# Optimization experiments

Measured on AMD Instinct MI355X. Metric: run time of the kernel, lower is better.

The kernel has to match this reference:

```python
import jax, jax.numpy as jnp
import numpy as np

B, T, C = 8, 2048, 1024


def setup_inputs() -> dict:
    key = jax.random.key(0)
    ks = jax.random.split(key, 7)
    s = 0.02  # typical init scale for weights
    return {
        "x": jax.random.normal(ks[0], (B, T, C), jnp.float32),
        "wq": jax.random.normal(ks[1], (C, C), jnp.float32) * s,
        "bq": jax.random.normal(ks[2], (C,), jnp.float32) * s,
        "wk": jax.random.normal(ks[3], (C, C), jnp.float32) * s,
        "bk": jax.random.normal(ks[4], (C,), jnp.float32) * s,
        "wv": jax.random.normal(ks[5], (C, C), jnp.float32) * s,
        "bv": jax.random.normal(ks[6], (C,), jnp.float32) * s,
    }


def reference(x, wq, bq, wk, bk, wv, bv):
    # x: [B, T, C]; torch Linear stores weight as [out, in] -> x @ W.T + b
    Bx, Tx, Cx = x.shape
    Q = x @ wq.T + bq  # [B, T, C]
    K = x @ wk.T + bk
    V = x @ wv.T + bv
    # NOTE: source computes K @ Q^T (keys index rows, queries index columns)
    scores = jnp.einsum("btc,bsc->bts", K, Q) / jnp.sqrt(jnp.float32(Cx))  # [B, T, T]
    causal = jnp.tril(jnp.ones((Tx, Tx), dtype=bool))  # mask==0 above diagonal
    scores = jnp.where(causal, scores, -jnp.inf)
    # torch masked_fill with a (1,1,T,T) mask broadcasts scores to (1,B,T,T)
    scores = scores[None]  # [1, B, T, T]
    w = jax.nn.softmax(scores, axis=-1)
    out = jnp.einsum("abts,bsc->abtc", w, V)  # [1, B, T, C]
    return out
```

## Files before the change

kernel.cpp:

```cpp
#include <hip/hip_runtime.h>
#include <stdint.h>

typedef unsigned short u16;
typedef __attribute__((ext_vector_type(8))) __bf16 bf16x8;
typedef __attribute__((ext_vector_type(4))) float f32x4;

#define DEVI __device__ __forceinline__

DEVI u16 f32_to_bf16(float f) {
  uint32_t u = __builtin_bit_cast(uint32_t, f);
  u += 0x7FFFu + ((u >> 16) & 1u);
  return (u16)(u >> 16);
}

DEVI void gl2lds16(const void* g, void* l) {
  __builtin_amdgcn_global_load_lds(
      (const __attribute__((address_space(1))) void*)g,
      (__attribute__((address_space(3))) void*)l, 16, 0, 0);
}

#define S_BATCH 2228224

__global__ void cast_f32_to_bf16_kernel(const float* __restrict__ src,
                                        u16* __restrict__ dst, int n4) {
  int i = blockIdx.x * blockDim.x + threadIdx.x;
  const int stride = gridDim.x * blockDim.x;
  for (; i < n4; i += stride) {
    const float4 v = ((const float4*)src)[i];
    ushort4 o;
    o.x = f32_to_bf16(v.x);
    o.y = f32_to_bf16(v.y);
    o.z = f32_to_bf16(v.z);
    o.w = f32_to_bf16(v.w);
    ((ushort4*)dst)[i] = o;
  }
}

__global__ void cast_w_kernel(const float* __restrict__ wq,
                              const float* __restrict__ wk,
                              const float* __restrict__ wv,
                              u16* __restrict__ wb, float* __restrict__ sums) {
  const int z = blockIdx.y;
  if (z == 3) {
    int i = blockIdx.x * blockDim.x + threadIdx.x;
    if (i < 4096) ((float4*)sums)[i] = (float4){0.f, 0.f, 0.f, 0.f};
    return;
  }
  const float* src = (z == 0) ? wq : (z == 1) ? wk : wv;
  u16* dst = wb + (size_t)z * 1048576;
  int i = blockIdx.x * blockDim.x + threadIdx.x;
  const int stride = gridDim.x * blockDim.x;
  for (; i < 262144; i += stride) {
    const float4 v = ((const float4*)src)[i];
    ushort4 o;
    o.x = f32_to_bf16(v.x);
    o.y = f32_to_bf16(v.y);
    o.z = f32_to_bf16(v.z);
    o.w = f32_to_bf16(v.w);
    ((ushort4*)dst)[i] = o;
  }
}

__global__ __launch_bounds__(512, 2) void qkv_kernel(
    const u16* __restrict__ xb, const u16* __restrict__ wb,
    const float* __restrict__ bq, const float* __restrict__ bk,
    const float* __restrict__ bv, u16* __restrict__ Qb, u16* __restrict__ Kb,
    u16* __restrict__ Vt) {
  __shared__ __align__(16) u16 lds[65536];

  const int id = blockIdx.x;
  const int wg = (id & 7) * 96 + (id >> 3);
  const int g = wg >> 3, u = wg & 7;
  const int z = g >> 5;
  const int tp = g & 31;
  const int tmt = tp * 2 + (u >> 2);
  const int tct = u & 3;

  int m0, n0;
  const u16* Aptr;
  const u16* Bptr;
  if (z < 2) {
    m0 = tct * 256;
    n0 = tmt * 256;
    Aptr = wb + (size_t)z * 1048576 + (size_t)m0 * 1024;
    Bptr = xb + (size_t)n0 * 1024;
  } else {
    m0 = tmt * 256;
    n0 = tct * 256;
    Aptr = xb + (size_t)m0 * 1024;
    Bptr = wb + (size_t)2 * 1048576 + (size_t)n0 * 1024;
  }

  const int tid = threadIdx.x;
  const int srow = tid >> 3;
  const int sgrp = ((tid & 7) - srow) & 7;
  const u16* Ag = Aptr + (size_t)srow * 1024 + sgrp * 8;
  const u16* Bg = Bptr + (size_t)srow * 1024 + sgrp * 8;
  char* ldsDst = (char*)lds + tid * 16;

#define ST_A0(kt) do { const u16* s_ = Ag + (kt) * 64;           char* d_ = ldsDst + (((kt) & 1) * 65536);         gl2lds16(s_, d_); gl2lds16(s_ + 65536, d_ + 8192); } while (0)
#define ST_A1(kt) do { const u16* s_ = Ag + 131072 + (kt) * 64;  char* d_ = ldsDst + (((kt) & 1) * 65536) + 16384; gl2lds16(s_, d_); gl2lds16(s_ + 65536, d_ + 8192); } while (0)
#define ST_B0(kt) do { const u16* s_ = Bg + (kt) * 64;           char* d_ = ldsDst + (((kt) & 1) * 65536) + 32768; gl2lds16(s_, d_); gl2lds16(s_ + 65536, d_ + 8192); } while (0)
#define ST_B1(kt) do { const u16* s_ = Bg + 131072 + (kt) * 64;  char* d_ = ldsDst + (((kt) & 1) * 65536) + 49152; gl2lds16(s_, d_); gl2lds16(s_ + 65536, d_ + 8192); } while (0)

  ST_A0(0); ST_B0(0); ST_B1(0); ST_A1(0);
  ST_A0(1); ST_B0(1); ST_B1(1);

  const int lane = tid & 63, wid = tid >> 6;
  const int wr = wid >> 2, wc = wid & 3;
  const int l15 = lane & 15, quad = lane >> 4;

  int aoff[4][2], boff[2][2];
#pragma unroll
  for (int i_ = 0; i_ < 4; ++i_) {
    const int arow = wr * 64 + i_ * 16 + l15;
#pragma unroll
    for (int k_ = 0; k_ < 2; ++k_)
      aoff[i_][k_] = arow * 64 + ((k_ * 4 + quad + arow) & 7) * 8;
  }
#pragma unroll
  for (int j_ = 0; j_ < 2; ++j_) {
    const int brow = wc * 32 + j_ * 16 + l15;
#pragma unroll
    for (int k_ = 0; k_ < 2; ++k_)
      boff[j_][k_] = brow * 64 + ((k_ * 4 + quad + brow) & 7) * 8;
  }

  f32x4 acc[2][2][4][2];
#pragma unroll
  for (int a_ = 0; a_ < 2; ++a_)
#pragma unroll
    for (int b_ = 0; b_ < 2; ++b_)
#pragma unroll
      for (int i_ = 0; i_ < 4; ++i_)
#pragma unroll
        for (int j_ = 0; j_ < 2; ++j_)
          acc[a_][b_][i_][j_] = (f32x4){0.f, 0.f, 0.f, 0.f};

  bf16x8 af[4][2], bfr[2][2][2];

#define LOADA(qm, buf) do { const u16* p_ = lds + (buf) * 32768 + (qm) * 8192; \
  _Pragma("unroll") for (int i_ = 0; i_ < 4; ++i_) \
  _Pragma("unroll") for (int k_ = 0; k_ < 2; ++k_) \
    af[i_][k_] = *(const bf16x8*)(p_ + aoff[i_][k_]); } while (0)
#define LOADB(qn, buf) do { const u16* p_ = lds + (buf) * 32768 + 16384 + (qn) * 8192; \
  _Pragma("unroll") for (int j_ = 0; j_ < 2; ++j_) \
  _Pragma("unroll") for (int k_ = 0; k_ < 2; ++k_) \
    bfr[qn][j_][k_] = *(const bf16x8*)(p_ + boff[j_][k_]); } while (0)
#define MMA(qm, qn) do { \
  _Pragma("unroll") for (int i_ = 0; i_ < 4; ++i_) \
  _Pragma("unroll") for (int j_ = 0; j_ < 2; ++j_) \
  _Pragma("unroll") for (int k_ = 0; k_ < 2; ++k_) \
    acc[qm][qn][i_][j_] = __builtin_amdgcn_mfma_f32_16x16x32_bf16( \
        af[i_][k_], bfr[qn][j_][k_], acc[qm][qn][i_][j_], 0, 0, 0); } while (0)

#define BAR __builtin_amdgcn_s_barrier()
#define WLG0 asm volatile("s_waitcnt lgkmcnt(0)")
#define WLG8 asm volatile("s_waitcnt lgkmcnt(8)")
#define PRIO1 __builtin_amdgcn_s_setprio(1)
#define PRIO0 __builtin_amdgcn_s_setprio(0)
#define WVM6 asm volatile("s_waitcnt vmcnt(6)" ::: "memory")
#define WVM0 asm volatile("s_waitcnt vmcnt(0)" ::: "memory")

  WVM6;
  BAR;

#pragma unroll 1
  for (int it = 0; it < 7; ++it) {
    const int j0 = 2 * it;
    LOADA(0, 0); LOADB(0, 0); ST_A1(j0 + 1); WLG8;
    BAR; WLG0; PRIO1; MMA(0, 0); PRIO0; BAR;
    LOADB(1, 0); ST_A0(j0 + 2);
    BAR; WLG0; PRIO1; MMA(0, 1); PRIO0; BAR;
    LOADA(1, 0); ST_B0(j0 + 2);
    BAR; WLG0; PRIO1; MMA(1, 1); PRIO0; BAR;
    ST_B1(j0 + 2);
    BAR; PRIO1; MMA(1, 0); PRIO0;
    WVM6;
    BAR;
    LOADA(0, 1); LOADB(0, 1); ST_A1(j0 + 2); WLG8;
    BAR; WLG0; PRIO1; MMA(0, 0); PRIO0; BAR;
    LOADB(1, 1); ST_A0(j0 + 3);
    BAR; WLG0; PRIO1; MMA(0, 1); PRIO0; BAR;
    LOADA(1, 1); ST_B0(j0 + 3);
    BAR; WLG0; PRIO1; MMA(1, 1); PRIO0; BAR;
    ST_B1(j0 + 3);
    BAR; PRIO1; MMA(1, 0); PRIO0;
    WVM6;
    BAR;
  }
  {
    LOADA(0, 0); LOADB(0, 0); ST_A1(15); WLG8;
    BAR; WLG0; PRIO1; MMA(0, 0); PRIO0; BAR;
    LOADB(1, 0);
    BAR; WLG0; PRIO1; MMA(0, 1); PRIO0; BAR;
    LOADA(1, 0);
    BAR; WLG0; PRIO1; MMA(1, 1); PRIO0; BAR;
    BAR; PRIO1; MMA(1, 0); PRIO0;
    WVM0;
    BAR;
    LOADA(0, 1); LOADB(0, 1); WLG8;
    BAR; WLG0; PRIO1; MMA(0, 0); PRIO0; BAR;
    LOADB(1, 1);
    BAR; WLG0; PRIO1; MMA(0, 1); PRIO0; BAR;
    LOADA(1, 1);
    BAR; WLG0; PRIO1; MMA(1, 1); PRIO0; BAR;
    PRIO1; MMA(1, 0); PRIO0;
    BAR;
  }

  if (z < 2) {
    const float* bias = (z == 0) ? bq : bk;
    u16* Out = (z == 0) ? Qb : Kb;
#pragma unroll
    for (int th = 0; th < 2; ++th) {
      if (th) __syncthreads();
#pragma unroll
      for (int qm = 0; qm < 2; ++qm)
#pragma unroll
        for (int i_ = 0; i_ < 4; ++i_) {
          const int c = qm * 128 + wr * 64 + i_ * 16 + quad * 4;
          const float4 b4 = *(const float4*)(bias + m0 + c);
#pragma unroll
          for (int j_ = 0; j_ < 2; ++j_) {
            const int row = wc * 32 + j_ * 16 + l15;
            ushort4 o;
            o.x = f32_to_bf16(acc[qm][th][i_][j_][0] + b4.x);
            o.y = f32_to_bf16(acc[qm][th][i_][j_][1] + b4.y);
            o.z = f32_to_bf16(acc[qm][th][i_][j_][2] + b4.z);
            o.w = f32_to_bf16(acc[qm][th][i_][j_][3] + b4.w);
            *(ushort4*)(lds + row * 264 + c) = o;
          }
        }
      __syncthreads();
#pragma unroll
      for (int p = 0; p < 8; ++p) {
        const int row = p * 16 + (tid >> 5);
        const int c0 = (tid & 31) * 8;
        const uint4 v = *(const uint4*)(lds + row * 264 + c0);
        *(uint4*)(Out + (size_t)(n0 + th * 128 + row) * 1024 + m0 + c0) = v;
      }
    }
  } else {
    const int b = m0 >> 11;
    const int t0b = m0 & 2047;
    u16* Out = Vt + (size_t)b * 2097152;
#pragma unroll
    for (int th = 0; th < 2; ++th) {
      if (th) __syncthreads();
#pragma unroll
      for (int j_ = 0; j_ < 2; ++j_) {
        const int row = wc * 32 + j_ * 16 + l15;
        const float bb = bv[n0 + th * 128 + row];
#pragma unroll
        for (int qm = 0; qm < 2; ++qm)
#pragma unroll
          for (int i_ = 0; i_ < 4; ++i_) {
            const int c = qm * 128 + wr * 64 + i_ * 16 + quad * 4;
            ushort4 o;
            o.x = f32_to_bf16(acc[qm][th][i_][j_][0] + bb);
            o.y = f32_to_bf16(acc[qm][th][i_][j_][1] + bb);
            o.z = f32_to_bf16(acc[qm][th][i_][j_][2] + bb);
            o.w = f32_to_bf16(acc[qm][th][i_][j_][3] + bb);
            *(ushort4*)(lds + row * 264 + c) = o;
          }
      }
      __syncthreads();
#pragma unroll
      for (int p = 0; p < 8; ++p) {
        const int row = p * 16 + (tid >> 5);
        const int c0 = (tid & 31) * 8;
        const uint4 v = *(const uint4*)(lds + row * 264 + c0);
        *(uint4*)(Out + (size_t)(n0 + th * 128 + row) * 2048 + t0b + c0) = v;
      }
    }
  }
#undef ST_A0
#undef ST_A1
#undef ST_B0
#undef ST_B1
#undef LOADA
#undef LOADB
#undef MMA
#undef BAR
#undef WLG0
#undef WLG8
#undef PRIO1
#undef PRIO0
#undef WVM6
#undef WVM0
}

__global__ __launch_bounds__(512, 2) void score_kernel(const u16* __restrict__ Kb,
                                                       const u16* __restrict__ Qb,
                                                       u16* __restrict__ Spk,
                                                       float* __restrict__ sums) {
  __shared__ __align__(16) u16 lds[49152];

  const int id = blockIdx.x;
  const int b = id & 7;
  const int l = id >> 3;
  int k = (int)((sqrtf(4.f * l + 1.f) - 1.f) * 0.5f);
  if (k * (k + 1) > l) --k;
  if ((k + 1) * (k + 2) <= l) ++k;
  const int off = l - k * (k + 1);
  const int hi = (off >= (k + 1));
  const int rt = 2 * k + hi;
  const int ct = off - (hi ? (k + 1) : 0);
  const bool maskT = (ct == k);

  const int tid = threadIdx.x;
  const int srow = tid >> 3;
  const int sgrp = ((tid & 7) - srow) & 7;
  const u16* A = Qb + ((size_t)b * 2048 + ct * 256) * 1024;
  const u16* B = Kb + ((size_t)b * 2048 + rt * 128) * 1024;
  const u16* Ag = A + (size_t)srow * 1024 + sgrp * 8;
  const u16* Bg = B + (size_t)srow * 1024 + sgrp * 8;
  char* ldsDst = (char*)lds + tid * 16;

#define ST_A0(kt) do { const u16* s_ = Ag + (kt) * 64;           char* d_ = ldsDst + (((kt) & 1) * 49152);         gl2lds16(s_, d_); gl2lds16(s_ + 65536, d_ + 8192); } while (0)
#define ST_A1(kt) do { const u16* s_ = Ag + 131072 + (kt) * 64;  char* d_ = ldsDst + (((kt) & 1) * 49152) + 16384; gl2lds16(s_, d_); gl2lds16(s_ + 65536, d_ + 8192); } while (0)
#define ST_B(kt)  do { const u16* s_ = Bg + (kt) * 64;           char* d_ = ldsDst + (((kt) & 1) * 49152) + 32768; gl2lds16(s_, d_); gl2lds16(s_ + 65536, d_ + 8192); } while (0)

  ST_A0(0); ST_B(0); ST_A1(0);
  ST_A0(1); ST_B(1);

  const int lane = tid & 63, wid = tid >> 6;
  const int wr = wid >> 2, wc = wid & 3;
  const int l15 = lane & 15, quad = lane >> 4;

  int aoff[4][2], boff[2][2];
#pragma unroll
  for (int i_ = 0; i_ < 4; ++i_) {
    const int arow = wr * 64 + i_ * 16 + l15;
#pragma unroll
    for (int k_ = 0; k_ < 2; ++k_)
      aoff[i_][k_] = arow * 64 + ((k_ * 4 + quad + arow) & 7) * 8;
  }
#pragma unroll
  for (int j_ = 0; j_ < 2; ++j_) {
    const int brow = wc * 32 + j_ * 16 + l15;
#pragma unroll
    for (int k_ = 0; k_ < 2; ++k_)
      boff[j_][k_] = brow * 64 + ((k_ * 4 + quad + brow) & 7) * 8;
  }

  f32x4 acc[2][4][2];
#pragma unroll
  for (int q_ = 0; q_ < 2; ++q_)
#pragma unroll
    for (int i_ = 0; i_ < 4; ++i_)
#pragma unroll
      for (int j_ = 0; j_ < 2; ++j_)
        acc[q_][i_][j_] = (f32x4){0.f, 0.f, 0.f, 0.f};

  bf16x8 af[4][2], bfr[2][2];

#define SLOADA(qm, buf) do { const u16* p_ = lds + (buf) * 24576 + (qm) * 8192; \
  _Pragma("unroll") for (int i_ = 0; i_ < 4; ++i_) \
  _Pragma("unroll") for (int k_ = 0; k_ < 2; ++k_) \
    af[i_][k_] = *(const bf16x8*)(p_ + aoff[i_][k_]); } while (0)
#define SLOADB(buf) do { const u16* p_ = lds + (buf) * 24576 + 16384; \
  _Pragma("unroll") for (int j_ = 0; j_ < 2; ++j_) \
  _Pragma("unroll") for (int k_ = 0; k_ < 2; ++k_) \
    bfr[j_][k_] = *(const bf16x8*)(p_ + boff[j_][k_]); } while (0)
#define SMMA(qm) do { \
  _Pragma("unroll") for (int i_ = 0; i_ < 4; ++i_) \
  _Pragma("unroll") for (int j_ = 0; j_ < 2; ++j_) \
  _Pragma("unroll") for (int k_ = 0; k_ < 2; ++k_) \
    acc[qm][i_][j_] = __builtin_amdgcn_mfma_f32_16x16x32_bf16( \
        af[i_][k_], bfr[j_][k_], acc[qm][i_][j_], 0, 0, 0); } while (0)

#define BAR __builtin_amdgcn_s_barrier()
#define WLG0 asm volatile("s_waitcnt lgkmcnt(0)")
#define PRIO1 __builtin_amdgcn_s_setprio(1)
#define PRIO0 __builtin_amdgcn_s_setprio(0)
#define WVM4 asm volatile("s_waitcnt vmcnt(4)" ::: "memory")
#define WVM0 asm volatile("s_waitcnt vmcnt(0)" ::: "memory")

  WVM4;
  BAR;

#pragma unroll 1
  for (int it = 0; it < 7; ++it) {
    const int j0 = 2 * it;
    SLOADA(0, 0); SLOADB(0); ST_A1(j0 + 1);
    BAR; WLG0; PRIO1; SMMA(0); PRIO0; BAR;
    SLOADA(1, 0); ST_A0(j0 + 2); ST_B(j0 + 2);
    BAR; WLG0; PRIO1; SMMA(1); PRIO0;
    WVM4;
    BAR;
    SLOADA(0, 1); SLOADB(1); ST_A1(j0 + 2);
    BAR; WLG0; PRIO1; SMMA(0); PRIO0; BAR;
    SLOADA(1, 1); ST_A0(j0 + 3); ST_B(j0 + 3);
    BAR; WLG0; PRIO1; SMMA(1); PRIO0;
    WVM4;
    BAR;
  }
  {
    SLOADA(0, 0); SLOADB(0); ST_A1(15);
    BAR; WLG0; PRIO1; SMMA(0); PRIO0; BAR;
    SLOADA(1, 0);
    BAR; WLG0; PRIO1; SMMA(1); PRIO0;
    WVM0;
    BAR;
    SLOADA(0, 1); SLOADB(1);
    BAR; WLG0; PRIO1; SMMA(0); PRIO0; BAR;
    SLOADA(1, 1);
    BAR; WLG0; PRIO1; SMMA(1); PRIO0; BAR;
  }

  const int moff = (rt & 1) * 128;
  float sj[2] = {0.f, 0.f};
#pragma unroll
  for (int qm = 0; qm < 2; ++qm)
#pragma unroll
    for (int i_ = 0; i_ < 4; ++i_) {
      const int s0 = qm * 128 + wr * 64 + i_ * 16 + quad * 4;
#pragma unroll
      for (int j_ = 0; j_ < 2; ++j_) {
        const int t = wc * 32 + j_ * 16 + l15;
        ushort4 o;
        float e[4];
#pragma unroll
        for (int r = 0; r < 4; ++r) {
          float v = __expf(acc[qm][i_][j_][r] * 0.03125f);
          if (maskT && (s0 + r) > (t + moff)) v = 0.f;
          e[r] = v;
          sj[j_] += v;
        }
        o.x = f32_to_bf16(e[0]);
        o.y = f32_to_bf16(e[1]);
        o.z = f32_to_bf16(e[2]);
        o.w = f32_to_bf16(e[3]);
        *(ushort4*)(lds + t * 264 + s0) = o;
      }
    }
#pragma unroll
  for (int j_ = 0; j_ < 2; ++j_) {
    float v = sj[j_];
    v += __shfl_xor(v, 16);
    v += __shfl_xor(v, 32);
    if (quad == 0)
      atomicAdd(&sums[(size_t)b * 2048 + rt * 128 + wc * 32 + j_ * 16 + l15], v);
  }
  __syncthreads();
  const int ld = (rt + 1) * 128;
  const int nc = ld - ct * 256;
  u16* Out = Spk + (size_t)b * S_BATCH + (size_t)(rt * (rt + 1) / 2) * 16384 +
             ct * 256;
  if (nc >= 256) {
#pragma unroll
    for (int p = 0; p < 8; ++p) {
      const int row = p * 16 + (tid >> 5);
      const int c0 = (tid & 31) * 8;
      const uint4 v = *(const uint4*)(lds + row * 264 + c0);
      *(uint4*)(Out + (size_t)row * ld + c0) = v;
    }
  } else {
#pragma unroll
    for (int p = 0; p < 4; ++p) {
      const int row = p * 32 + (tid >> 4);
      const int c0 = (tid & 15) * 8;
      const uint4 v = *(const uint4*)(lds + row * 264 + c0);
      *(uint4*)(Out + (size_t)row * ld + c0) = v;
    }
  }
#undef ST_A0
#undef ST_A1
#undef ST_B
#undef SLOADA
#undef SLOADB
#undef SMMA
#undef BAR
#undef WLG0
#undef PRIO1
#undef PRIO0
#undef WVM4
#undef WVM0
}

__global__ __launch_bounds__(512, 2) void pv_kernel(const u16* __restrict__ Spk,
                                                    const u16* __restrict__ Vt,
                                                    const float* __restrict__ sums,
                                                    float* __restrict__ Out) {
  __shared__ __align__(16) u16 lds[49152];

  const int id = blockIdx.x;
  const int hf = id >> 8;
  const int rr_ = id & 255;
  const int rt = hf ? (rr_ >> 5) : 15 - (rr_ >> 5);
  const int ct = (rr_ >> 3) & 3;
  const int b = rr_ & 7;

  const int ldb = (rt + 1) * 128;
  const int nk2 = rt + 1;

  const int tid = threadIdx.x;
  const int srow = tid >> 3;
  const int sgrp = ((tid & 7) - srow) & 7;
  const u16* A = Vt + ((size_t)b * 1024 + ct * 256) * 2048;
  const u16* B = Spk + (size_t)b * S_BATCH +
                 (size_t)(rt * (rt + 1) / 2) * 16384;
  const u16* Ag = A + (size_t)srow * 2048 + sgrp * 8;
  const u16* Bg = B + (size_t)srow * ldb + sgrp * 8;
  char* ldsDst = (char*)lds + tid * 16;

#define ST_A0(kt) do { const u16* s_ = Ag + (kt) * 64;            char* d_ = ldsDst + (((kt) & 1) * 49152);         gl2lds16(s_, d_); gl2lds16(s_ + 131072, d_ + 8192); } while (0)
#define ST_A1(kt) do { const u16* s_ = Ag + 262144 + (kt) * 64;   char* d_ = ldsDst + (((kt) & 1) * 49152) + 16384; gl2lds16(s_, d_); gl2lds16(s_ + 131072, d_ + 8192); } while (0)
#define ST_B(kt)  do { const u16* s_ = Bg + (kt) * 64;            char* d_ = ldsDst + (((kt) & 1) * 49152) + 32768; gl2lds16(s_, d_); gl2lds16(s_ + (size_t)64 * ldb, d_ + 8192); } while (0)

  ST_A0(0); ST_B(0); ST_A1(0);
  ST_A0(1); ST_B(1);

  const int lane = tid & 63, wid = tid >> 6;
  const int wr = wid >> 2, wc = wid & 3;
  const int l15 = lane & 15, quad = lane >> 4;

  int aoff[4][2], boff[2][2];
#pragma unroll
  for (int i_ = 0; i_ < 4; ++i_) {
    const int arow = wr * 64 + i_ * 16 + l15;
#pragma unroll
    for (int k_ = 0; k_ < 2; ++k_)
      aoff[i_][k_] = arow * 64 + ((k_ * 4 + quad + arow) & 7) * 8;
  }
#pragma unroll
  for (int j_ = 0; j_ < 2; ++j_) {
    const int brow = wc * 32 + j_ * 16 + l15;
#pragma unroll
    for (int k_ = 0; k_ < 2; ++k_)
      boff[j_][k_] = brow * 64 + ((k_ * 4 + quad + brow) & 7) * 8;
  }

  f32x4 acc[2][4][2];
#pragma unroll
  for (int q_ = 0; q_ < 2; ++q_)
#pragma unroll
    for (int i_ = 0; i_ < 4; ++i_)
#pragma unroll
      for (int j_ = 0; j_ < 2; ++j_)
        acc[q_][i_][j_] = (f32x4){0.f, 0.f, 0.f, 0.f};

  bf16x8 af[4][2], bfr[2][2];

#define SLOADA(qm, buf) do { const u16* p_ = lds + (buf) * 24576 + (qm) * 8192; \
  _Pragma("unroll") for (int i_ = 0; i_ < 4; ++i_) \
  _Pragma("unroll") for (int k_ = 0; k_ < 2; ++k_) \
    af[i_][k_] = *(const bf16x8*)(p_ + aoff[i_][k_]); } while (0)
#define SLOADB(buf) do { const u16* p_ = lds + (buf) * 24576 + 16384; \
  _Pragma("unroll") for (int j_ = 0; j_ < 2; ++j_) \
  _Pragma("unroll") for (int k_ = 0; k_ < 2; ++k_) \
    bfr[j_][k_] = *(const bf16x8*)(p_ + boff[j_][k_]); } while (0)
#define SMMA(qm) do { \
  _Pragma("unroll") for (int i_ = 0; i_ < 4; ++i_) \
  _Pragma("unroll") for (int j_ = 0; j_ < 2; ++j_) \
  _Pragma("unroll") for (int k_ = 0; k_ < 2; ++k_) \
    acc[qm][i_][j_] = __builtin_amdgcn_mfma_f32_16x16x32_bf16( \
        af[i_][k_], bfr[j_][k_], acc[qm][i_][j_], 0, 0, 0); } while (0)

#define BAR __builtin_amdgcn_s_barrier()
#define WLG0 asm volatile("s_waitcnt lgkmcnt(0)")
#define PRIO1 __builtin_amdgcn_s_setprio(1)
#define PRIO0 __builtin_amdgcn_s_setprio(0)
#define WVM4 asm volatile("s_waitcnt vmcnt(4)" ::: "memory")
#define WVM0 asm volatile("s_waitcnt vmcnt(0)" ::: "memory")

  WVM4;
  BAR;

#pragma unroll 1
  for (int it = 0; it < nk2 - 1; ++it) {
    const int j0 = 2 * it;
    SLOADA(0, 0); SLOADB(0); ST_A1(j0 + 1);
    BAR; WLG0; PRIO1; SMMA(0); PRIO0; BAR;
    SLOADA(1, 0); ST_A0(j0 + 2); ST_B(j0 + 2);
    BAR; WLG0; PRIO1; SMMA(1); PRIO0;
    WVM4;
    BAR;
    SLOADA(0, 1); SLOADB(1); ST_A1(j0 + 2);
    BAR; WLG0; PRIO1; SMMA(0); PRIO0; BAR;
    SLOADA(1, 1); ST_A0(j0 + 3); ST_B(j0 + 3);
    BAR; WLG0; PRIO1; SMMA(1); PRIO0;
    WVM4;
    BAR;
  }
  {
    SLOADA(0, 0); SLOADB(0); ST_A1(2 * nk2 - 1);
    BAR; WLG0; PRIO1; SMMA(0); PRIO0; BAR;
    SLOADA(1, 0);
    BAR; WLG0; PRIO1; SMMA(1); PRIO0;
    WVM0;
    BAR;
    SLOADA(0, 1); SLOADB(1);
    BAR; WLG0; PRIO1; SMMA(0); PRIO0; BAR;
    SLOADA(1, 1);
    BAR; WLG0; PRIO1; SMMA(1); PRIO0; BAR;
  }

  float* ftile = (float*)lds;
  const float* sumsb = sums + (size_t)b * 2048 + rt * 128;
  float* Ob = Out + (size_t)b * 2048 * 1024 + (size_t)(rt * 128) * 1024 +
              ct * 256;
  float iv[2];
#pragma unroll
  for (int j_ = 0; j_ < 2; ++j_)
    iv[j_] = 1.0f / sumsb[wc * 32 + j_ * 16 + l15];
#pragma unroll
  for (int qm = 0; qm < 2; ++qm) {
    if (qm) __syncthreads();
#pragma unroll
    for (int i_ = 0; i_ < 4; ++i_) {
      const int c0 = wr * 64 + i_ * 16 + quad * 4;
#pragma unroll
      for (int j_ = 0; j_ < 2; ++j_) {
        const int t = wc * 32 + j_ * 16 + l15;
        float4 v;
        v.x = acc[qm][i_][j_][0] * iv[j_];
        v.y = acc[qm][i_][j_][1] * iv[j_];
        v.z = acc[qm][i_][j_][2] * iv[j_];
        v.w = acc[qm][i_][j_][3] * iv[j_];
        *(float4*)(ftile + t * 132 + c0) = v;
      }
    }
    __syncthreads();
#pragma unroll
    for (int p = 0; p < 8; ++p) {
      const int row = p * 16 + (tid >> 5);
      const int c0f = (tid & 31) * 4;
      const float4 v = *(const float4*)(ftile + row * 132 + c0f);
      *(float4*)(Ob + (size_t)row * 1024 + qm * 128 + c0f) = v;
    }
  }
#undef ST_A0
#undef ST_A1
#undef ST_B
#undef SLOADA
#undef SLOADB
#undef SMMA
#undef BAR
#undef WLG0
#undef PRIO1
#undef PRIO0
#undef WVM4
#undef WVM0
}

extern "C" void kernel_launch(void* const* d_in, const int* in_sizes, int n_in,
                              void* d_out, int out_size, void* d_ws,
                              size_t ws_size, hipStream_t stream) {
  const float* x = (const float*)d_in[0];
  const float* wq = (const float*)d_in[1];
  const float* bq = (const float*)d_in[2];
  const float* wk = (const float*)d_in[3];
  const float* bk = (const float*)d_in[4];
  const float* wv = (const float*)d_in[5];
  const float* bv = (const float*)d_in[6];
  float* out = (float*)d_out;
  char* ws = (char*)d_ws;

  u16* Qb = (u16*)(ws);
  u16* Kb = (u16*)(ws + ((size_t)32 << 20));
  u16* Vt = (u16*)(ws + ((size_t)64 << 20));
  u16* Spk = (u16*)(ws + ((size_t)96 << 20));
  u16* xb = (u16*)(ws + ((size_t)96 << 20));
  float* sums = (float*)(ws + ((size_t)132 << 20));
  u16* wb = (u16*)(ws + ((size_t)134 << 20));

  cast_f32_to_bf16_kernel<<<16384, 256, 0, stream>>>(x, xb, 16777216 / 4);
  cast_w_kernel<<<dim3(512, 4), 256, 0, stream>>>(wq, wk, wv, wb, sums);

  qkv_kernel<<<768, 512, 0, stream>>>(xb, wb, bq, bk, bv, Qb, Kb, Vt);

  score_kernel<<<576, 512, 0, stream>>>(Kb, Qb, Spk, sums);

  pv_kernel<<<512, 512, 0, stream>>>(Spk, Vt, sums, out);
}
```

Before: 331.8 us.

## Compute Q, K, V projections in one persistent block per tile

The QKV kernel now launches one block per (token tile, channel tile) instead of one per projection. Each block loops over Q, K and V in turn, reusing the same x panel and prefetching the next projection's first k-tiles while the previous result is written back through a swizzled LDS staging area. This cuts launch count and overlaps the epilogue with the next GEMM's loads, at the cost of a third as many blocks, which may leave CUs underused on a 256-CU part. The pv_kernel row-tile ordering for its second half is also reversed to pair long and short tiles.

```diff
diff --git a/kernel.cpp b/kernel.cpp
--- a/kernel.cpp
+++ b/kernel.cpp
@@ -69,42 +69,30 @@
   __shared__ __align__(16) u16 lds[65536];
 
   const int id = blockIdx.x;
-  const int wg = (id & 7) * 96 + (id >> 3);
-  const int g = wg >> 3, u = wg & 7;
-  const int z = g >> 5;
-  const int tp = g & 31;
-  const int tmt = tp * 2 + (u >> 2);
-  const int tct = u & 3;
-
-  int m0, n0;
-  const u16* Aptr;
-  const u16* Bptr;
-  if (z < 2) {
-    m0 = tct * 256;
-    n0 = tmt * 256;
-    Aptr = wb + (size_t)z * 1048576 + (size_t)m0 * 1024;
-    Bptr = xb + (size_t)n0 * 1024;
-  } else {
-    m0 = tmt * 256;
-    n0 = tct * 256;
-    Aptr = xb + (size_t)m0 * 1024;
-    Bptr = wb + (size_t)2 * 1048576 + (size_t)n0 * 1024;
-  }
+  const int xcd = id & 7;
+  const int local = id >> 3;
+  const int tct = local & 3;
+  const int tmt = xcd * 8 + (local >> 2);
 
   const int tid = threadIdx.x;
   const int srow = tid >> 3;
   const int sgrp = ((tid & 7) - srow) & 7;
-  const u16* Ag = Aptr + (size_t)srow * 1024 + sgrp * 8;
-  const u16* Bg = Bptr + (size_t)srow * 1024 + sgrp * 8;
   char* ldsDst = (char*)lds + tid * 16;
 
-#define ST_A0(kt) do { const u16* s_ = Ag + (kt) * 64;           char* d_ = ldsDst + (((kt) & 1) * 65536);         gl2lds16(s_, d_); gl2lds16(s_ + 65536, d_ + 8192); } while (0)
-#define ST_A1(kt) do { const u16* s_ = Ag + 131072 + (kt) * 64;  char* d_ = ldsDst + (((kt) & 1) * 65536) + 16384; gl2lds16(s_, d_); gl2lds16(s_ + 65536, d_ + 8192); } while (0)
-#define ST_B0(kt) do { const u16* s_ = Bg + (kt) * 64;           char* d_ = ldsDst + (((kt) & 1) * 65536) + 32768; gl2lds16(s_, d_); gl2lds16(s_ + 65536, d_ + 8192); } while (0)
-#define ST_B1(kt) do { const u16* s_ = Bg + 131072 + (kt) * 64;  char* d_ = ldsDst + (((kt) & 1) * 65536) + 49152; gl2lds16(s_, d_); gl2lds16(s_ + 65536, d_ + 8192); } while (0)
-
-  ST_A0(0); ST_B0(0); ST_B1(0); ST_A1(0);
-  ST_A0(1); ST_B0(1); ST_B1(1);
+  const size_t rowoff = (size_t)srow * 1024 + sgrp * 8;
+  const u16* xpan = xb + (size_t)(tmt * 256) * 1024 + rowoff;
+  const u16* wpanQ = wb + (size_t)(tct * 256) * 1024 + rowoff;
+  const u16* wpanK = wpanQ + 1048576;
+  const u16* wpanV = wpanQ + 2097152;
+
+#define STN_A0(ag, kt) do { const u16* s_ = (ag) + (kt) * 64;           char* d_ = ldsDst + (((kt) & 1) * 65536);         gl2lds16(s_, d_); gl2lds16(s_ + 65536, d_ + 8192); } while (0)
+#define STN_A1(ag, kt) do { const u16* s_ = (ag) + 131072 + (kt) * 64;  char* d_ = ldsDst + (((kt) & 1) * 65536) + 16384; gl2lds16(s_, d_); gl2lds16(s_ + 65536, d_ + 8192); } while (0)
+#define STN_B0(bg, kt) do { const u16* s_ = (bg) + (kt) * 64;           char* d_ = ldsDst + (((kt) & 1) * 65536) + 32768; gl2lds16(s_, d_); gl2lds16(s_ + 65536, d_ + 8192); } while (0)
+#define STN_B1(bg, kt) do { const u16* s_ = (bg) + 131072 + (kt) * 64;  char* d_ = ldsDst + (((kt) & 1) * 65536) + 49152; gl2lds16(s_, d_); gl2lds16(s_ + 65536, d_ + 8192); } while (0)
+#define ST_A0(kt) STN_A0(agCur, kt)
+#define ST_A1(kt) STN_A1(agCur, kt)
+#define ST_B0(kt) STN_B0(bgCur, kt)
+#define ST_B1(kt) STN_B1(bgCur, kt)
 
   const int lane = tid & 63, wid = tid >> 6;
   const int wr = wid >> 2, wc = wid & 3;
@@ -127,16 +115,6 @@
   }
 
   f32x4 acc[2][2][4][2];
-#pragma unroll
-  for (int a_ = 0; a_ < 2; ++a_)
-#pragma unroll
-    for (int b_ = 0; b_ < 2; ++b_)
-#pragma unroll
-      for (int i_ = 0; i_ < 4; ++i_)
-#pragma unroll
-        for (int j_ = 0; j_ < 2; ++j_)
-          acc[a_][b_][i_][j_] = (f32x4){0.f, 0.f, 0.f, 0.f};
-
   bf16x8 af[4][2], bfr[2][2][2];
 
 #define LOADA(qm, buf) do { const u16* p_ = lds + (buf) * 32768 + (qm) * 8192; \
@@ -160,88 +138,129 @@
 #define PRIO1 __builtin_amdgcn_s_setprio(1)
 #define PRIO0 __builtin_amdgcn_s_setprio(0)
 #define WVM6 asm volatile("s_waitcnt vmcnt(6)" ::: "memory")
+#define WVM22 asm volatile("s_waitcnt vmcnt(22)" ::: "memory")
 #define WVM0 asm volatile("s_waitcnt vmcnt(0)" ::: "memory")
-
+#define FENCE asm volatile("" ::: "memory")
+
+  const u16* agCur = wpanQ;
+  const u16* bgCur = xpan;
+  int m0 = tct * 256, n0 = tmt * 256;
+
+  ST_A0(0); ST_B0(0); ST_B1(0); ST_A1(0);
+  ST_A0(1); ST_B0(1); ST_B1(1);
   WVM6;
   BAR;
 
 #pragma unroll 1
-  for (int it = 0; it < 7; ++it) {
-    const int j0 = 2 * it;
-    LOADA(0, 0); LOADB(0, 0); ST_A1(j0 + 1); WLG8;
-    BAR; WLG0; PRIO1; MMA(0, 0); PRIO0; BAR;
-    LOADB(1, 0); ST_A0(j0 + 2);
-    BAR; WLG0; PRIO1; MMA(0, 1); PRIO0; BAR;
-    LOADA(1, 0); ST_B0(j0 + 2);
-    BAR; WLG0; PRIO1; MMA(1, 1); PRIO0; BAR;
-    ST_B1(j0 + 2);
-    BAR; PRIO1; MMA(1, 0); PRIO0;
-    WVM6;
-    BAR;
-    LOADA(0, 1); LOADB(0, 1); ST_A1(j0 + 2); WLG8;
-    BAR; WLG0; PRIO1; MMA(0, 0); PRIO0; BAR;
-    LOADB(1, 1); ST_A0(j0 + 3);
-    BAR; WLG0; PRIO1; MMA(0, 1); PRIO0; BAR;
-    LOADA(1, 1); ST_B0(j0 + 3);
-    BAR; WLG0; PRIO1; MMA(1, 1); PRIO0; BAR;
-    ST_B1(j0 + 3);
-    BAR; PRIO1; MMA(1, 0); PRIO0;
-    WVM6;
-    BAR;
-  }
-  {
-    LOADA(0, 0); LOADB(0, 0); ST_A1(15); WLG8;
-    BAR; WLG0; PRIO1; MMA(0, 0); PRIO0; BAR;
-    LOADB(1, 0);
-    BAR; WLG0; PRIO1; MMA(0, 1); PRIO0; BAR;
-    LOADA(1, 0);
-    BAR; WLG0; PRIO1; MMA(1, 1); PRIO0; BAR;
-    BAR; PRIO1; MMA(1, 0); PRIO0;
-    WVM0;
-    BAR;
-    LOADA(0, 1); LOADB(0, 1); WLG8;
-    BAR; WLG0; PRIO1; MMA(0, 0); PRIO0; BAR;
-    LOADB(1, 1);
-    BAR; WLG0; PRIO1; MMA(0, 1); PRIO0; BAR;
-    LOADA(1, 1);
-    BAR; WLG0; PRIO1; MMA(1, 1); PRIO0; BAR;
-    PRIO1; MMA(1, 0); PRIO0;
-    BAR;
-  }
-
-  if (z < 2) {
-    const float* bias = (z == 0) ? bq : bk;
-    u16* Out = (z == 0) ? Qb : Kb;
-#pragma unroll
-    for (int th = 0; th < 2; ++th) {
-      if (th) __syncthreads();
-#pragma unroll
-      for (int qm = 0; qm < 2; ++qm)
-#pragma unroll
-        for (int i_ = 0; i_ < 4; ++i_) {
-          const int c = qm * 128 + wr * 64 + i_ * 16 + quad * 4;
-          const float4 b4 = *(const float4*)(bias + m0 + c);
-#pragma unroll
-          for (int j_ = 0; j_ < 2; ++j_) {
-            const int row = wc * 32 + j_ * 16 + l15;
-            ushort4 o;
-            o.x = f32_to_bf16(acc[qm][th][i_][j_][0] + b4.x);
-            o.y = f32_to_bf16(acc[qm][th][i_][j_][1] + b4.y);
-            o.z = f32_to_bf16(acc[qm][th][i_][j_][2] + b4.z);
-            o.w = f32_to_bf16(acc[qm][th][i_][j_][3] + b4.w);
-            *(ushort4*)(lds + row * 264 + c) = o;
+  for (int z = 0; z < 3; ++z) {
+#pragma unroll
+    for (int a_ = 0; a_ < 2; ++a_)
+#pragma unroll
+      for (int b_ = 0; b_ < 2; ++b_)
+#pragma unroll
+        for (int i_ = 0; i_ < 4; ++i_)
+#pragma unroll
+          for (int j_ = 0; j_ < 2; ++j_)
+            acc[a_][b_][i_][j_] = (f32x4){0.f, 0.f, 0.f, 0.f};
+
+#pragma unroll 1
+    for (int it = 0; it < 7; ++it) {
+      const int j0 = 2 * it;
+      LOADA(0, 0); LOADB(0, 0); ST_A1(j0 + 1); WLG8;
+      BAR; WLG0; PRIO1; MMA(0, 0); PRIO0; BAR;
+      LOADB(1, 0); ST_A0(j0 + 2);
+      BAR; WLG0; PRIO1; MMA(0, 1); PRIO0; BAR;
+      LOADA(1, 0); ST_B0(j0 + 2);
+      BAR; WLG0; PRIO1; MMA(1, 1); PRIO0; BAR;
+      ST_B1(j0 + 2);
+      BAR; PRIO1; MMA(1, 0); PRIO0;
+      WVM6;
+      BAR;
+      LOADA(0, 1); LOADB(0, 1); ST_A1(j0 + 2); WLG8;
+      BAR; WLG0; PRIO1; MMA(0, 0); PRIO0; BAR;
+      LOADB(1, 1); ST_A0(j0 + 3);
+      BAR; WLG0; PRIO1; MMA(0, 1); PRIO0; BAR;
+      LOADA(1, 1); ST_B0(j0 + 3);
+      BAR; WLG0; PRIO1; MMA(1, 1); PRIO0; BAR;
+      ST_B1(j0 + 3);
+      BAR; PRIO1; MMA(1, 0); PRIO0;
+      WVM6;
+      BAR;
+    }
+    {
+      LOADA(0, 0); LOADB(0, 0); ST_A1(15); WLG8;
+      BAR; WLG0; PRIO1; MMA(0, 0); PRIO0; BAR;
+      LOADB(1, 0);
+      BAR; WLG0; PRIO1; MMA(0, 1); PRIO0; BAR;
+      LOADA(1, 0);
+      BAR; WLG0; PRIO1; MMA(1, 1); PRIO0; BAR;
+      BAR; PRIO1; MMA(1, 0); PRIO0;
+      WVM0;
+      BAR;
+      LOADA(0, 1); LOADB(0, 1); WLG8;
+      BAR; WLG0; PRIO1; MMA(0, 0); PRIO0; BAR;
+      LOADB(1, 1);
+      BAR; WLG0; PRIO1; MMA(0, 1); PRIO0; BAR;
+      LOADA(1, 1);
+      BAR; WLG0; PRIO1; MMA(1, 1); PRIO0; BAR;
+      PRIO1; MMA(1, 0); PRIO0;
+      BAR;
+    }
+
+    if (z < 3 - 1) {
+      const u16* agN = (z == 0) ? wpanK : xpan;
+      const u16* bgN = (z == 0) ? xpan : wpanV;
+      FENCE;
+      STN_A0(agN, 0); STN_B0(bgN, 0); STN_B1(bgN, 0); STN_A1(agN, 0);
+      FENCE;
+      {
+        u16* stg = lds + 32768;
+        const float* bias = (z == 0) ? bq : bk;
+        u16* Out = (z == 0) ? Qb : Kb;
+#pragma unroll
+        for (int th = 0; th < 2; ++th) {
+          if (th) { WLG0; BAR; }
+#pragma unroll
+          for (int qm = 0; qm < 2; ++qm)
+#pragma unroll
+            for (int i_ = 0; i_ < 4; ++i_) {
+              const int c = qm * 128 + wr * 64 + i_ * 16 + quad * 4;
+              const float4 b4 = *(const float4*)(bias + m0 + c);
+#pragma unroll
+              for (int j_ = 0; j_ < 2; ++j_) {
+                const int row = wc * 32 + j_ * 16 + l15;
+                ushort4 o;
+                o.x = f32_to_bf16(acc[qm][th][i_][j_][0] + b4.x);
+                o.y = f32_to_bf16(acc[qm][th][i_][j_][1] + b4.y);
+                o.z = f32_to_bf16(acc[qm][th][i_][j_][2] + b4.z);
+                o.w = f32_to_bf16(acc[qm][th][i_][j_][3] + b4.w);
+                *(ushort4*)(stg + row * 256 + ((c + row * 8) & 255)) = o;
+              }
+            }
+          WLG0; BAR;
+#pragma unroll
+          for (int p = 0; p < 8; ++p) {
+            const int row = p * 16 + (tid >> 5);
+            const int c0 = (tid & 31) * 8;
+            const uint4 v =
+                *(const uint4*)(stg + row * 256 + ((c0 + row * 8) & 255));
+            *(uint4*)(Out + (size_t)(n0 + th * 128 + row) * 1024 + m0 + c0) = v;
           }
         }
-      __syncthreads();
-#pragma unroll
-      for (int p = 0; p < 8; ++p) {
-        const int row = p * 16 + (tid >> 5);
-        const int c0 = (tid & 31) * 8;
-        const uint4 v = *(const uint4*)(lds + row * 264 + c0);
-        *(uint4*)(Out + (size_t)(n0 + th * 128 + row) * 1024 + m0 + c0) = v;
+        WLG0; BAR;
       }
-    }
-  } else {
+      FENCE;
+      STN_A0(agN, 1); STN_B0(bgN, 1); STN_B1(bgN, 1);
+      WVM22;
+      BAR;
+      agCur = agN;
+      bgCur = bgN;
+      m0 = (z == 0) ? tct * 256 : tmt * 256;
+      n0 = (z == 0) ? tmt * 256 : tct * 256;
+    }
+  }
+
+  {
     const int b = m0 >> 11;
     const int t0b = m0 & 2047;
     u16* Out = Vt + (size_t)b * 2097152;
@@ -275,6 +294,10 @@
       }
     }
   }
+#undef STN_A0
+#undef STN_A1
+#undef STN_B0
+#undef STN_B1
 #undef ST_A0
 #undef ST_A1
 #undef ST_B0
@@ -288,7 +311,9 @@
 #undef PRIO1
 #undef PRIO0
 #undef WVM6
+#undef WVM22
 #undef WVM0
+#undef FENCE
 }
 
 __global__ __launch_bounds__(512, 2) void score_kernel(const u16* __restrict__ Kb,
@@ -489,7 +514,7 @@
   const int id = blockIdx.x;
   const int hf = id >> 8;
   const int rr_ = id & 255;
-  const int rt = hf ? (rr_ >> 5) : 15 - (rr_ >> 5);
+  const int rt = (hf ? 7 : 15) - (rr_ >> 5);
   const int ct = (rr_ >> 3) & 3;
   const int b = rr_ & 7;
 
@@ -670,7 +695,7 @@
   cast_f32_to_bf16_kernel<<<16384, 256, 0, stream>>>(x, xb, 16777216 / 4);
   cast_w_kernel<<<dim3(512, 4), 256, 0, stream>>>(wq, wk, wv, wb, sums);
 
-  qkv_kernel<<<768, 512, 0, stream>>>(xb, wb, bq, bk, bv, Qb, Kb, Vt);
+  qkv_kernel<<<256, 512, 0, stream>>>(xb, wb, bq, bk, bv, Qb, Kb, Vt);
 
   score_kernel<<<576, 512, 0, stream>>>(Kb, Qb, Spk, sums);
 
```

New measurement: 329.8 us. Within noise of the previous version (-0.6%).

## Single-buffer B tile in score and PV kernels to raise occupancy

Applied to the files above, without the earlier changes.

Restructures the LDS pipeline in the score and PV GEMM kernels so the B operand is single-buffered and the A halves are double-buffered separately. This cuts shared memory per block from 96KB to 80KB. Launch bounds are raised to allow more blocks per CU, and the global-to-LDS issue order and vmcnt waits are adjusted to match. The aim is more resident blocks to hide latency, at the cost of tighter register limits and less prefetch depth for B.

```diff
diff --git a/kernel.cpp b/kernel.cpp
--- a/kernel.cpp
+++ b/kernel.cpp
@@ -291,11 +291,11 @@
 #undef WVM0
 }
 
-__global__ __launch_bounds__(512, 2) void score_kernel(const u16* __restrict__ Kb,
+__global__ __launch_bounds__(512, 4) void score_kernel(const u16* __restrict__ Kb,
                                                        const u16* __restrict__ Qb,
                                                        u16* __restrict__ Spk,
                                                        float* __restrict__ sums) {
-  __shared__ __align__(16) u16 lds[49152];
+  __shared__ __align__(16) u16 lds[40960];
 
   const int id = blockIdx.x;
   const int b = id & 7;
@@ -318,12 +318,11 @@
   const u16* Bg = B + (size_t)srow * 1024 + sgrp * 8;
   char* ldsDst = (char*)lds + tid * 16;
 
-#define ST_A0(kt) do { const u16* s_ = Ag + (kt) * 64;           char* d_ = ldsDst + (((kt) & 1) * 49152);         gl2lds16(s_, d_); gl2lds16(s_ + 65536, d_ + 8192); } while (0)
-#define ST_A1(kt) do { const u16* s_ = Ag + 131072 + (kt) * 64;  char* d_ = ldsDst + (((kt) & 1) * 49152) + 16384; gl2lds16(s_, d_); gl2lds16(s_ + 65536, d_ + 8192); } while (0)
-#define ST_B(kt)  do { const u16* s_ = Bg + (kt) * 64;           char* d_ = ldsDst + (((kt) & 1) * 49152) + 32768; gl2lds16(s_, d_); gl2lds16(s_ + 65536, d_ + 8192); } while (0)
-
-  ST_A0(0); ST_B(0); ST_A1(0);
-  ST_A0(1); ST_B(1);
+#define ST_A0(kt) do { const u16* s_ = Ag + (kt) * 64;           char* d_ = ldsDst + (((kt) & 1) * 16384);         gl2lds16(s_, d_); gl2lds16(s_ + 65536, d_ + 8192); } while (0)
+#define ST_A1(kt) do { const u16* s_ = Ag + 131072 + (kt) * 64;  char* d_ = ldsDst + 32768 + (((kt) & 1) * 16384); gl2lds16(s_, d_); gl2lds16(s_ + 65536, d_ + 8192); } while (0)
+#define ST_B(kt)  do { const u16* s_ = Bg + (kt) * 64;           char* d_ = ldsDst + 65536;                        gl2lds16(s_, d_); gl2lds16(s_ + 65536, d_ + 8192); } while (0)
+
+  ST_A0(0); ST_B(0); ST_A1(0); ST_A0(1);
 
   const int lane = tid & 63, wid = tid >> 6;
   const int wr = wid >> 2, wc = wid & 3;
@@ -356,11 +355,11 @@
 
   bf16x8 af[4][2], bfr[2][2];
 
-#define SLOADA(qm, buf) do { const u16* p_ = lds + (buf) * 24576 + (qm) * 8192; \
+#define SLOADA(qm, buf) do { const u16* p_ = lds + (qm) * 16384 + (buf) * 8192; \
   _Pragma("unroll") for (int i_ = 0; i_ < 4; ++i_) \
   _Pragma("unroll") for (int k_ = 0; k_ < 2; ++k_) \
     af[i_][k_] = *(const bf16x8*)(p_ + aoff[i_][k_]); } while (0)
-#define SLOADB(buf) do { const u16* p_ = lds + (buf) * 24576 + 16384; \
+#define SLOADB do { const u16* p_ = lds + 32768; \
   _Pragma("unroll") for (int j_ = 0; j_ < 2; ++j_) \
   _Pragma("unroll") for (int k_ = 0; k_ < 2; ++k_) \
     bfr[j_][k_] = *(const bf16x8*)(p_ + boff[j_][k_]); } while (0)
@@ -375,36 +374,36 @@
 #define WLG0 asm volatile("s_waitcnt lgkmcnt(0)")
 #define PRIO1 __builtin_amdgcn_s_setprio(1)
 #define PRIO0 __builtin_amdgcn_s_setprio(0)
-#define WVM4 asm volatile("s_waitcnt vmcnt(4)" ::: "memory")
+#define WVM2 asm volatile("s_waitcnt vmcnt(2)" ::: "memory")
 #define WVM0 asm volatile("s_waitcnt vmcnt(0)" ::: "memory")
 
-  WVM4;
+  WVM2;
   BAR;
 
 #pragma unroll 1
   for (int it = 0; it < 7; ++it) {
     const int j0 = 2 * it;
-    SLOADA(0, 0); SLOADB(0); ST_A1(j0 + 1);
-    BAR; WLG0; PRIO1; SMMA(0); PRIO0; BAR;
-    SLOADA(1, 0); ST_A0(j0 + 2); ST_B(j0 + 2);
+    SLOADA(0, 0); SLOADB; ST_A1(j0 + 1);
+    BAR; WLG0; PRIO1; SMMA(0); PRIO0; BAR;
+    SLOADA(1, 0); ST_B(j0 + 1); ST_A0(j0 + 2);
     BAR; WLG0; PRIO1; SMMA(1); PRIO0;
-    WVM4;
-    BAR;
-    SLOADA(0, 1); SLOADB(1); ST_A1(j0 + 2);
-    BAR; WLG0; PRIO1; SMMA(0); PRIO0; BAR;
-    SLOADA(1, 1); ST_A0(j0 + 3); ST_B(j0 + 3);
+    WVM2;
+    BAR;
+    SLOADA(0, 1); SLOADB; ST_A1(j0 + 2);
+    BAR; WLG0; PRIO1; SMMA(0); PRIO0; BAR;
+    SLOADA(1, 1); ST_B(j0 + 2); ST_A0(j0 + 3);
     BAR; WLG0; PRIO1; SMMA(1); PRIO0;
-    WVM4;
+    WVM2;
     BAR;
   }
   {
-    SLOADA(0, 0); SLOADB(0); ST_A1(15);
-    BAR; WLG0; PRIO1; SMMA(0); PRIO0; BAR;
-    SLOADA(1, 0);
+    SLOADA(0, 0); SLOADB; ST_A1(15);
+    BAR; WLG0; PRIO1; SMMA(0); PRIO0; BAR;
+    SLOADA(1, 0); ST_B(15);
     BAR; WLG0; PRIO1; SMMA(1); PRIO0;
     WVM0;
     BAR;
-    SLOADA(0, 1); SLOADB(1);
+    SLOADA(0, 1); SLOADB;
     BAR; WLG0; PRIO1; SMMA(0); PRIO0; BAR;
     SLOADA(1, 1);
     BAR; WLG0; PRIO1; SMMA(1); PRIO0; BAR;
@@ -476,15 +475,15 @@
 #undef WLG0
 #undef PRIO1
 #undef PRIO0
-#undef WVM4
+#undef WVM2
 #undef WVM0
 }
 
-__global__ __launch_bounds__(512, 2) void pv_kernel(const u16* __restrict__ Spk,
+__global__ __launch_bounds__(512, 4) void pv_kernel(const u16* __restrict__ Spk,
                                                     const u16* __restrict__ Vt,
                                                     const float* __restrict__ sums,
                                                     float* __restrict__ Out) {
-  __shared__ __align__(16) u16 lds[49152];
+  __shared__ __align__(16) u16 lds[40960];
 
   const int id = blockIdx.x;
   const int hf = id >> 8;
@@ -506,12 +505,11 @@
   const u16* Bg = B + (size_t)srow * ldb + sgrp * 8;
   char* ldsDst = (char*)lds + tid * 16;
 
-#define ST_A0(kt) do { const u16* s_ = Ag + (kt) * 64;            char* d_ = ldsDst + (((kt) & 1) * 49152);         gl2lds16(s_, d_); gl2lds16(s_ + 131072, d_ + 8192); } while (0)
-#define ST_A1(kt) do { const u16* s_ = Ag + 262144 + (kt) * 64;   char* d_ = ldsDst + (((kt) & 1) * 49152) + 16384; gl2lds16(s_, d_); gl2lds16(s_ + 131072, d_ + 8192); } while (0)
-#define ST_B(kt)  do { const u16* s_ = Bg + (kt) * 64;            char* d_ = ldsDst + (((kt) & 1) * 49152) + 32768; gl2lds16(s_, d_); gl2lds16(s_ + (size_t)64 * ldb, d_ + 8192); } while (0)
-
-  ST_A0(0); ST_B(0); ST_A1(0);
-  ST_A0(1); ST_B(1);
+#define ST_A0(kt) do { const u16* s_ = Ag + (kt) * 64;            char* d_ = ldsDst + (((kt) & 1) * 16384);         gl2lds16(s_, d_); gl2lds16(s_ + 131072, d_ + 8192); } while (0)
+#define ST_A1(kt) do { const u16* s_ = Ag + 262144 + (kt) * 64;   char* d_ = ldsDst + 32768 + (((kt) & 1) * 16384); gl2lds16(s_, d_); gl2lds16(s_ + 131072, d_ + 8192); } while (0)
+#define ST_B(kt)  do { const u16* s_ = Bg + (kt) * 64;            char* d_ = ldsDst + 65536;                        gl2lds16(s_, d_); gl2lds16(s_ + (size_t)64 * ldb, d_ + 8192); } while (0)
+
+  ST_A0(0); ST_B(0); ST_A1(0); ST_A0(1);
 
   const int lane = tid & 63, wid = tid >> 6;
   const int wr = wid >> 2, wc = wid & 3;
@@ -544,11 +542,11 @@
 
   bf16x8 af[4][2], bfr[2][2];
 
-#define SLOADA(qm, buf) do { const u16* p_ = lds + (buf) * 24576 + (qm) * 8192; \
+#define SLOADA(qm, buf) do { const u16* p_ = lds + (qm) * 16384 + (buf) * 8192; \
   _Pragma("unroll") for (int i_ = 0; i_ < 4; ++i_) \
   _Pragma("unroll") for (int k_ = 0; k_ < 2; ++k_) \
     af[i_][k_] = *(const bf16x8*)(p_ + aoff[i_][k_]); } while (0)
-#define SLOADB(buf) do { const u16* p_ = lds + (buf) * 24576 + 16384; \
+#define SLOADB do { const u16* p_ = lds + 32768; \
   _Pragma("unroll") for (int j_ = 0; j_ < 2; ++j_) \
   _Pragma("unroll") for (int k_ = 0; k_ < 2; ++k_) \
     bfr[j_][k_] = *(const bf16x8*)(p_ + boff[j_][k_]); } while (0)
@@ -563,36 +561,36 @@
 #define WLG0 asm volatile("s_waitcnt lgkmcnt(0)")
 #define PRIO1 __builtin_amdgcn_s_setprio(1)
 #define PRIO0 __builtin_amdgcn_s_setprio(0)
-#define WVM4 asm volatile("s_waitcnt vmcnt(4)" ::: "memory")
+#define WVM2 asm volatile("s_waitcnt vmcnt(2)" ::: "memory")
 #define WVM0 asm volatile("s_waitcnt vmcnt(0)" ::: "memory")
 
-  WVM4;
+  WVM2;
   BAR;
 
 #pragma unroll 1
   for (int it = 0; it < nk2 - 1; ++it) {
     const int j0 = 2 * it;
-    SLOADA(0, 0); SLOADB(0); ST_A1(j0 + 1);
-    BAR; WLG0; PRIO1; SMMA(0); PRIO0; BAR;
-    SLOADA(1, 0); ST_A0(j0 + 2); ST_B(j0 + 2);
+    SLOADA(0, 0); SLOADB; ST_A1(j0 + 1);
+    BAR; WLG0; PRIO1; SMMA(0); PRIO0; BAR;
+    SLOADA(1, 0); ST_B(j0 + 1); ST_A0(j0 + 2);
     BAR; WLG0; PRIO1; SMMA(1); PRIO0;
-    WVM4;
-    BAR;
-    SLOADA(0, 1); SLOADB(1); ST_A1(j0 + 2);
-    BAR; WLG0; PRIO1; SMMA(0); PRIO0; BAR;
-    SLOADA(1, 1); ST_A0(j0 + 3); ST_B(j0 + 3);
+    WVM2;
+    BAR;
+    SLOADA(0, 1); SLOADB; ST_A1(j0 + 2);
+    BAR; WLG0; PRIO1; SMMA(0); PRIO0; BAR;
+    SLOADA(1, 1); ST_B(j0 + 2); ST_A0(j0 + 3);
     BAR; WLG0; PRIO1; SMMA(1); PRIO0;
-    WVM4;
+    WVM2;
     BAR;
   }
   {
-    SLOADA(0, 0); SLOADB(0); ST_A1(2 * nk2 - 1);
-    BAR; WLG0; PRIO1; SMMA(0); PRIO0; BAR;
-    SLOADA(1, 0);
+    SLOADA(0, 0); SLOADB; ST_A1(2 * nk2 - 1);
+    BAR; WLG0; PRIO1; SMMA(0); PRIO0; BAR;
+    SLOADA(1, 0); ST_B(2 * nk2 - 1);
     BAR; WLG0; PRIO1; SMMA(1); PRIO0;
     WVM0;
     BAR;
-    SLOADA(0, 1); SLOADB(1);
+    SLOADA(0, 1); SLOADB;
     BAR; WLG0; PRIO1; SMMA(0); PRIO0; BAR;
     SLOADA(1, 1);
     BAR; WLG0; PRIO1; SMMA(1); PRIO0; BAR;
@@ -642,7 +640,7 @@
 #undef WLG0
 #undef PRIO1
 #undef PRIO0
-#undef WVM4
+#undef WVM2
 #undef WVM0
 }
 
```

Measured after the change: 361.4 us. 1.09x slower.
